# Performance work log

Measured on AMD Instinct MI355X. Metric: run time of the kernel, lower is better.

Reference implementation:

```python
import jax, jax.numpy as jnp
import numpy as np

N_NODES = 20000
N_EDGES = 640000
D = 128


def setup_inputs() -> dict:
    key = jax.random.key(0)
    ks = jax.random.split(key, 8)
    scale = 1.0 / np.sqrt(D)
    x = jax.random.normal(ks[0], (N_NODES, D), dtype=jnp.float32)
    edge_index = jax.random.randint(ks[1], (2, N_EDGES), 0, N_NODES, dtype=jnp.int64)
    W1_rel = jax.random.normal(ks[2], (D, D), dtype=jnp.float32) * scale
    b1_rel = jnp.zeros((D,), dtype=jnp.float32)
    W1_root = jax.random.normal(ks[3], (D, D), dtype=jnp.float32) * scale
    W2_rel = jax.random.normal(ks[4], (D, D), dtype=jnp.float32) * scale
    b2_rel = jnp.zeros((D,), dtype=jnp.float32)
    W2_root = jax.random.normal(ks[5], (D, D), dtype=jnp.float32) * scale
    return {"x": x, "edge_index": edge_index,
            "W1_rel": W1_rel, "b1_rel": b1_rel, "W1_root": W1_root,
            "W2_rel": W2_rel, "b2_rel": b2_rel, "W2_root": W2_root}


def _graph_conv(x, src, dst, W_rel, b_rel, W_root):
    # sum-aggregate neighbor features: gather from src, scatter-add to dst
    agg = jax.ops.segment_sum(x[src], dst, num_segments=N_NODES)  # [N, D]
    # PyG GraphConv: lin_rel(agg) (with bias) + lin_root(x) (no bias)
    return agg @ W_rel + b_rel + x @ W_root


def reference(x, edge_index, W1_rel, b1_rel, W1_root, W2_rel, b2_rel, W2_root):
    src, dst = edge_index[0], edge_index[1]  # messages flow src (j) -> dst (i)
    h = jax.nn.relu(_graph_conv(x, src, dst, W1_rel, b1_rel, W1_root))
    out = _graph_conv(h, src, dst, W2_rel, b2_rel, W2_root)  # final ReLU stripped
    return out
```

## Files before the change

### kernel.cpp

```cpp
#include <hip/hip_runtime.h>

#define N_NODES 20000
#define N_EDGES 640000
#define D 128
#define CAP 128

typedef __attribute__((ext_vector_type(8))) short bf16x8;
typedef __attribute__((ext_vector_type(4))) float f32x4;

__device__ __forceinline__ short f2bf(float f) {
    union { float f; unsigned u; } un; un.f = f;
    unsigned r = un.u + 0x7fff + ((un.u >> 16) & 1);
    return (short)(r >> 16);
}
__device__ __forceinline__ float bflo(unsigned u) {
    return __uint_as_float(u << 16);
}
__device__ __forceinline__ float bfhi(unsigned u) {
    return __uint_as_float(u & 0xffff0000u);
}

__global__ __launch_bounds__(256) void fill_kernel(
    const int* __restrict__ src, const int* __restrict__ dst,
    int* __restrict__ cnt, int* __restrict__ buckets)
{
    int i = blockIdx.x * 256 + threadIdx.x;
    if (i < N_EDGES) {
        int d = dst[i];
        int p = atomicAdd(&cnt[d], 1);
        if (p < CAP) buckets[(d << 7) + p] = src[i];
    }
}

__global__ __launch_bounds__(256) void convert_kernel(
    const float* __restrict__ in, short* __restrict__ out)
{
    int i = blockIdx.x * 256 + threadIdx.x;
    float4 v = ((const float4*)in)[i];
    ushort4 o;
    o.x = (unsigned short)f2bf(v.x);
    o.y = (unsigned short)f2bf(v.y);
    o.z = (unsigned short)f2bf(v.z);
    o.w = (unsigned short)f2bf(v.w);
    ((ushort4*)out)[i] = o;
}

__global__ __launch_bounds__(256) void pack_w_kernel(
    const float* __restrict__ Wrel, const float* __restrict__ Wroot,
    short* __restrict__ Wpk)
{
    int idx = blockIdx.x * 256 + threadIdx.x;
    int lane = idx & 63;
    int ct   = (idx >> 6) & 7;
    int t    = idx >> 9;
    const float* W = (t < 4) ? Wrel : Wroot;
    int k0  = (t & 3) * 32 + (lane >> 4) * 8;
    int col = ct * 16 + (lane & 15);
    short v[8];
#pragma unroll
    for (int j = 0; j < 8; j++)
        v[j] = f2bf(W[(size_t)(k0 + j) * D + col]);
    bf16x8 pk;
#pragma unroll
    for (int j = 0; j < 8; j++) pk[j] = v[j];
    ((bf16x8*)Wpk)[idx] = pk;
}

__global__ __launch_bounds__(256) void aggregate_kernel(
    const short* __restrict__ xb,
    const int* __restrict__ cnt,
    const int* __restrict__ buckets,
    short* __restrict__ aggb)
{
    int node = blockIdx.x * 8 + (threadIdx.x >> 5);
    int lane = threadIdx.x & 31;
    int n = cnt[node];
    n = (n > CAP) ? CAP : n;
    const int* bl = buckets + (node << 7);

    float4 acc = make_float4(0.f, 0.f, 0.f, 0.f);
    int i = 0;
    for (; i + 8 <= n; i += 8) {
        uint2 u[8];
#pragma unroll
        for (int q = 0; q < 8; q++) {
            int s = bl[i + q];
            u[q] = *(const uint2*)(xb + (size_t)s * D + lane * 4);
        }
#pragma unroll
        for (int q = 0; q < 8; q++) {
            acc.x += bflo(u[q].x); acc.y += bfhi(u[q].x);
            acc.z += bflo(u[q].y); acc.w += bfhi(u[q].y);
        }
    }
    for (; i < n; i++) {
        int s = bl[i];
        uint2 uq = *(const uint2*)(xb + (size_t)s * D + lane * 4);
        acc.x += bflo(uq.x); acc.y += bfhi(uq.x);
        acc.z += bflo(uq.y); acc.w += bfhi(uq.y);
    }
    ushort4 o;
    o.x = (unsigned short)f2bf(acc.x);
    o.y = (unsigned short)f2bf(acc.y);
    o.z = (unsigned short)f2bf(acc.z);
    o.w = (unsigned short)f2bf(acc.w);
    *(ushort4*)(aggb + (size_t)node * D + lane * 4) = o;
}

template <bool RELU, bool OUT_BF16>
__global__ __launch_bounds__(128) void gemm_kernel(
    const short* __restrict__ aggb,
    const short* __restrict__ xb,
    const short* __restrict__ Wpk,
    const float* __restrict__ brel,
    void* __restrict__ outp)
{
    const int tid  = threadIdx.x;
    const int wave = tid >> 6;
    const int lane = tid & 63;
    const int quad = lane >> 4;
    const int l16  = lane & 15;
    const int row0 = blockIdx.x * 32 + wave * 16;

    f32x4 acc[8];
#pragma unroll
    for (int ct = 0; ct < 8; ct++) acc[ct] = (f32x4){0.f, 0.f, 0.f, 0.f};

    const short* arow_agg = aggb + (size_t)(row0 + l16) * D + quad * 8;
    const short* arow_x   = xb   + (size_t)(row0 + l16) * D + quad * 8;
    const bf16x8* wb = (const bf16x8*)Wpk + lane;

#pragma unroll
    for (int t = 0; t < 8; t++) {
        const short* arow = (t < 4) ? arow_agg : arow_x;
        const int k0 = (t & 3) * 32;
        bf16x8 a = *(const bf16x8*)(arow + k0);
        const bf16x8* wt = wb + (size_t)t * 8 * 64;
#pragma unroll
        for (int ct = 0; ct < 8; ct++) {
            bf16x8 b = wt[ct * 64];
            acc[ct] = __builtin_amdgcn_mfma_f32_16x16x32_bf16(a, b, acc[ct], 0, 0, 0);
        }
    }

    const int orow = row0 + quad * 4;
#pragma unroll
    for (int ct = 0; ct < 8; ct++) {
        const int col = ct * 16 + l16;
        const float bias = brel[col];
#pragma unroll
        for (int r = 0; r < 4; r++) {
            float v = acc[ct][r] + bias;
            if (RELU) v = fmaxf(v, 0.f);
            if (OUT_BF16)
                ((short*)outp)[(size_t)(orow + r) * D + col] = f2bf(v);
            else
                ((float*)outp)[(size_t)(orow + r) * D + col] = v;
        }
    }
}

extern "C" void kernel_launch(void* const* d_in, const int* in_sizes, int n_in,
                              void* d_out, int out_size, void* d_ws, size_t ws_size,
                              hipStream_t stream) {
    const float* x       = (const float*)d_in[0];
    const int*   ei      = (const int*)  d_in[1];
    const float* W1_rel  = (const float*)d_in[2];
    const float* b1_rel  = (const float*)d_in[3];
    const float* W1_root = (const float*)d_in[4];
    const float* W2_rel  = (const float*)d_in[5];
    const float* b2_rel  = (const float*)d_in[6];
    const float* W2_root = (const float*)d_in[7];
    float* out = (float*)d_out;

    char* p = (char*)d_ws;
    short* xb   = (short*)p;  p += (size_t)N_NODES * D * 2;
    short* hb   = (short*)p;  p += (size_t)N_NODES * D * 2;
    short* aggb = (short*)p;  p += (size_t)N_NODES * D * 2;
    short* wpk1 = (short*)p;  p += 65536;
    short* wpk2 = (short*)p;  p += 65536;
    int*   cnt  = (int*)p;    p += (size_t)N_NODES * 4;
    int*   buckets = (int*)p;

    const int* src = ei;
    const int* dst = ei + N_EDGES;

    const int eblocks   = (N_EDGES + 255) / 256;
    const int cblocks   = (N_NODES * D / 4) / 256;
    const int aggblocks = N_NODES / 8;
    const int gemmblocks = N_NODES / 32;

    hipMemsetAsync(cnt, 0, (size_t)N_NODES * sizeof(int), stream);
    fill_kernel<<<eblocks, 256, 0, stream>>>(src, dst, cnt, buckets);
    convert_kernel<<<cblocks, 256, 0, stream>>>(x, xb);
    pack_w_kernel<<<16, 256, 0, stream>>>(W1_rel, W1_root, wpk1);
    pack_w_kernel<<<16, 256, 0, stream>>>(W2_rel, W2_root, wpk2);

    aggregate_kernel<<<aggblocks, 256, 0, stream>>>(xb, cnt, buckets, aggb);
    gemm_kernel<true, true><<<gemmblocks, 128, 0, stream>>>(
        aggb, xb, wpk1, b1_rel, (void*)hb);

    aggregate_kernel<<<aggblocks, 256, 0, stream>>>(hb, cnt, buckets, aggb);
    gemm_kernel<false, false><<<gemmblocks, 128, 0, stream>>>(
        aggb, hb, wpk2, b2_rel, (void*)out);
}
```

Before: 178.1 us.

## Merge prep kernels into one launch and split edge buckets into four atomic slices

Replaces the edge-fill, feature-convert and two weight-pack kernels with a single block-partitioned prep kernel, removing three launches. Each destination node's bucket is split into four sub-slices of 32 with separate counters, selected by thread index, to spread atomic contention on hot nodes. The aggregate kernel reads the four counters with one vector load and walks each slice with a 4-way unrolled gather. Per-slice capacity of 32 means a node whose edges pile into one slice can drop edges that the old 128 capacity kept. Random degrees average 32 per node, so this truncation could affect correctness.

New measurement: 184.6 us. +3.7%, slower.

```diff
diff --git a/kernel.cpp b/kernel.cpp
--- a/kernel.cpp
+++ b/kernel.cpp
@@ -3,7 +3,8 @@
 #define N_NODES 20000
 #define N_EDGES 640000
 #define D 128
-#define CAP 128
+#define NSLICE 4
+#define SCAP 32
 
 typedef __attribute__((ext_vector_type(8))) short bf16x8;
 typedef __attribute__((ext_vector_type(4))) float f32x4;
@@ -13,57 +14,53 @@
     unsigned r = un.u + 0x7fff + ((un.u >> 16) & 1);
     return (short)(r >> 16);
 }
-__device__ __forceinline__ float bflo(unsigned u) {
-    return __uint_as_float(u << 16);
-}
-__device__ __forceinline__ float bfhi(unsigned u) {
-    return __uint_as_float(u & 0xffff0000u);
-}
-
-__global__ __launch_bounds__(256) void fill_kernel(
+__device__ __forceinline__ float bflo(unsigned u) { return __uint_as_float(u << 16); }
+__device__ __forceinline__ float bfhi(unsigned u) { return __uint_as_float(u & 0xffff0000u); }
+
+__global__ __launch_bounds__(256) void prep_kernel(
+    const float* __restrict__ x,
     const int* __restrict__ src, const int* __restrict__ dst,
-    int* __restrict__ cnt, int* __restrict__ buckets)
+    const float* __restrict__ W1_rel, const float* __restrict__ W1_root,
+    const float* __restrict__ W2_rel, const float* __restrict__ W2_root,
+    int* __restrict__ cnt, int* __restrict__ buckets,
+    short* __restrict__ xb, short* __restrict__ wpk1, short* __restrict__ wpk2)
 {
-    int i = blockIdx.x * 256 + threadIdx.x;
-    if (i < N_EDGES) {
+    const int b = blockIdx.x;
+    const int tid = threadIdx.x;
+    if (b < 2500) {
+        int i = b * 256 + tid;
         int d = dst[i];
-        int p = atomicAdd(&cnt[d], 1);
-        if (p < CAP) buckets[(d << 7) + p] = src[i];
-    }
-}
-
-__global__ __launch_bounds__(256) void convert_kernel(
-    const float* __restrict__ in, short* __restrict__ out)
-{
-    int i = blockIdx.x * 256 + threadIdx.x;
-    float4 v = ((const float4*)in)[i];
-    ushort4 o;
-    o.x = (unsigned short)f2bf(v.x);
-    o.y = (unsigned short)f2bf(v.y);
-    o.z = (unsigned short)f2bf(v.z);
-    o.w = (unsigned short)f2bf(v.w);
-    ((ushort4*)out)[i] = o;
-}
-
-__global__ __launch_bounds__(256) void pack_w_kernel(
-    const float* __restrict__ Wrel, const float* __restrict__ Wroot,
-    short* __restrict__ Wpk)
-{
-    int idx = blockIdx.x * 256 + threadIdx.x;
-    int lane = idx & 63;
-    int ct   = (idx >> 6) & 7;
-    int t    = idx >> 9;
-    const float* W = (t < 4) ? Wrel : Wroot;
-    int k0  = (t & 3) * 32 + (lane >> 4) * 8;
-    int col = ct * 16 + (lane & 15);
-    short v[8];
-#pragma unroll
-    for (int j = 0; j < 8; j++)
-        v[j] = f2bf(W[(size_t)(k0 + j) * D + col]);
-    bf16x8 pk;
-#pragma unroll
-    for (int j = 0; j < 8; j++) pk[j] = v[j];
-    ((bf16x8*)Wpk)[idx] = pk;
+        int s = tid & (NSLICE - 1);
+        int p = atomicAdd(&cnt[d * NSLICE + s], 1);
+        if (p < SCAP) buckets[(d << 7) + s * SCAP + p] = src[i];
+    } else if (b < 5000) {
+        int i = (b - 2500) * 256 + tid;
+        float4 v = ((const float4*)x)[i];
+        ushort4 o;
+        o.x = (unsigned short)f2bf(v.x);
+        o.y = (unsigned short)f2bf(v.y);
+        o.z = (unsigned short)f2bf(v.z);
+        o.w = (unsigned short)f2bf(v.w);
+        ((ushort4*)xb)[i] = o;
+    } else {
+        int pb  = b - 5000;
+        int job = pb >> 4;
+        int idx = (pb & 15) * 256 + tid;
+        const float* Wrel  = job ? W2_rel  : W1_rel;
+        const float* Wroot = job ? W2_root : W1_root;
+        short* Wpk = job ? wpk2 : wpk1;
+        int lane = idx & 63;
+        int ct   = (idx >> 6) & 7;
+        int t    = idx >> 9;
+        const float* W = (t < 4) ? Wrel : Wroot;
+        int k0  = (t & 3) * 32 + (lane >> 4) * 8;
+        int col = ct * 16 + (lane & 15);
+        bf16x8 pk;
+#pragma unroll
+        for (int j = 0; j < 8; j++)
+            pk[j] = f2bf(W[(size_t)(k0 + j) * D + col]);
+        ((bf16x8*)Wpk)[idx] = pk;
+    }
 }
 
 __global__ __launch_bounds__(256) void aggregate_kernel(
@@ -74,30 +71,33 @@
 {
     int node = blockIdx.x * 8 + (threadIdx.x >> 5);
     int lane = threadIdx.x & 31;
-    int n = cnt[node];
-    n = (n > CAP) ? CAP : n;
+    uint4 c4 = *(const uint4*)(cnt + node * NSLICE);
     const int* bl = buckets + (node << 7);
 
     float4 acc = make_float4(0.f, 0.f, 0.f, 0.f);
-    int i = 0;
-    for (; i + 8 <= n; i += 8) {
-        uint2 u[8];
-#pragma unroll
-        for (int q = 0; q < 8; q++) {
-            int s = bl[i + q];
-            u[q] = *(const uint2*)(xb + (size_t)s * D + lane * 4);
-        }
-#pragma unroll
-        for (int q = 0; q < 8; q++) {
-            acc.x += bflo(u[q].x); acc.y += bfhi(u[q].x);
-            acc.z += bflo(u[q].y); acc.w += bfhi(u[q].y);
-        }
-    }
-    for (; i < n; i++) {
-        int s = bl[i];
-        uint2 uq = *(const uint2*)(xb + (size_t)s * D + lane * 4);
-        acc.x += bflo(uq.x); acc.y += bfhi(uq.x);
-        acc.z += bflo(uq.y); acc.w += bfhi(uq.y);
+#pragma unroll
+    for (int s = 0; s < NSLICE; s++) {
+        int n = (int)((&c4.x)[s]);
+        n = (n > SCAP) ? SCAP : n;
+        const int* seg = bl + s * SCAP;
+        int i = 0;
+        for (; i + 4 <= n; i += 4) {
+            int s0 = seg[i + 0], s1 = seg[i + 1], s2 = seg[i + 2], s3 = seg[i + 3];
+            uint2 u0 = *(const uint2*)(xb + (size_t)s0 * D + lane * 4);
+            uint2 u1 = *(const uint2*)(xb + (size_t)s1 * D + lane * 4);
+            uint2 u2 = *(const uint2*)(xb + (size_t)s2 * D + lane * 4);
+            uint2 u3 = *(const uint2*)(xb + (size_t)s3 * D + lane * 4);
+            acc.x += bflo(u0.x) + bflo(u1.x) + bflo(u2.x) + bflo(u3.x);
+            acc.y += bfhi(u0.x) + bfhi(u1.x) + bfhi(u2.x) + bfhi(u3.x);
+            acc.z += bflo(u0.y) + bflo(u1.y) + bflo(u2.y) + bflo(u3.y);
+            acc.w += bfhi(u0.y) + bfhi(u1.y) + bfhi(u2.y) + bfhi(u3.y);
+        }
+        for (; i < n; i++) {
+            int s0 = seg[i];
+            uint2 u0 = *(const uint2*)(xb + (size_t)s0 * D + lane * 4);
+            acc.x += bflo(u0.x); acc.y += bfhi(u0.x);
+            acc.z += bflo(u0.y); acc.w += bfhi(u0.y);
+        }
     }
     ushort4 o;
     o.x = (unsigned short)f2bf(acc.x);
@@ -133,13 +133,12 @@
 #pragma unroll
     for (int t = 0; t < 8; t++) {
         const short* arow = (t < 4) ? arow_agg : arow_x;
-        const int k0 = (t & 3) * 32;
-        bf16x8 a = *(const bf16x8*)(arow + k0);
+        bf16x8 a = *(const bf16x8*)(arow + (t & 3) * 32);
         const bf16x8* wt = wb + (size_t)t * 8 * 64;
 #pragma unroll
         for (int ct = 0; ct < 8; ct++) {
-            bf16x8 b = wt[ct * 64];
-            acc[ct] = __builtin_amdgcn_mfma_f32_16x16x32_bf16(a, b, acc[ct], 0, 0, 0);
+            bf16x8 bfr = wt[ct * 64];
+            acc[ct] = __builtin_amdgcn_mfma_f32_16x16x32_bf16(a, bfr, acc[ct], 0, 0, 0);
         }
     }
 
@@ -179,22 +178,19 @@
     short* aggb = (short*)p;  p += (size_t)N_NODES * D * 2;
     short* wpk1 = (short*)p;  p += 65536;
     short* wpk2 = (short*)p;  p += 65536;
-    int*   cnt  = (int*)p;    p += (size_t)N_NODES * 4;
+    int*   cnt  = (int*)p;    p += (size_t)N_NODES * NSLICE * 4;
     int*   buckets = (int*)p;
 
     const int* src = ei;
     const int* dst = ei + N_EDGES;
 
-    const int eblocks   = (N_EDGES + 255) / 256;
-    const int cblocks   = (N_NODES * D / 4) / 256;
-    const int aggblocks = N_NODES / 8;
+    const int aggblocks  = N_NODES / 8;
     const int gemmblocks = N_NODES / 32;
 
-    hipMemsetAsync(cnt, 0, (size_t)N_NODES * sizeof(int), stream);
-    fill_kernel<<<eblocks, 256, 0, stream>>>(src, dst, cnt, buckets);
-    convert_kernel<<<cblocks, 256, 0, stream>>>(x, xb);
-    pack_w_kernel<<<16, 256, 0, stream>>>(W1_rel, W1_root, wpk1);
-    pack_w_kernel<<<16, 256, 0, stream>>>(W2_rel, W2_root, wpk2);
+    hipMemsetAsync(cnt, 0, (size_t)N_NODES * NSLICE * sizeof(int), stream);
+    prep_kernel<<<5032, 256, 0, stream>>>(
+        x, src, dst, W1_rel, W1_root, W2_rel, W2_root,
+        cnt, buckets, xb, wpk1, wpk2);
 
     aggregate_kernel<<<aggblocks, 256, 0, stream>>>(xb, cnt, buckets, aggb);
     gemm_kernel<true, true><<<gemmblocks, 128, 0, stream>>>(
```
